# Kernel optimization log

Measured on AMD Instinct MI355X. Metric: run time of the kernel, lower is better.

The kernel has to match this reference:

```python
import jax, jax.numpy as jnp
import numpy as np

EPS = 1e-12  # torch F.normalize eps


def setup_inputs() -> dict:
    key = jax.random.key(0)
    k1, k2, k3, k4, k5 = jax.random.split(key, 5)
    N, C, H, W = 32, 512, 32, 32
    E = 1024   # expansion * dim
    G = 8      # group
    D = E // G # 128, per-group channel dim
    K = 64     # num_clusters
    x = jax.random.normal(k1, (N, C, H, W), dtype=jnp.float32)
    W1 = jax.random.normal(k2, (E, C), dtype=jnp.float32) / np.sqrt(C)
    W2 = jax.random.normal(k3, (G, E), dtype=jnp.float32) / np.sqrt(E)
    Wc = jax.random.normal(k4, (K, D), dtype=jnp.float32) / np.sqrt(D)
    centroids = jax.random.uniform(k5, (K, D), dtype=jnp.float32)
    return {"x": x, "W1": W1, "W2": W2, "Wc": Wc, "centroids": centroids}


def reference(x, W1, W2, Wc, centroids):
    # x: [N, C, H, W]; W1: [E, C]; W2: [G, E]; Wc: [K, D]; centroids: [K, D]
    N, C, H, W = x.shape
    E = W1.shape[0]
    G = W2.shape[0]
    K, D = Wc.shape
    P = H * W
    # descriptor-wise L2 normalization over channel dim
    norm = jnp.linalg.norm(x, axis=1, keepdims=True)
    x = x / jnp.maximum(norm, EPS)
    # linear1 on channels: [N, E, P]
    xe = jnp.einsum('ncp,ec->nep', x.reshape(N, C, P), W1)
    # grouped features: [N, G, D, P]
    xg = xe.reshape(N, G, D, P)
    # attention gate: sigmoid(linear2)  -> [N, G, P]
    att = jax.nn.sigmoid(jnp.einsum('nep,ge->ngp', xe, W2))
    # 1x1 conv = per-pixel matmul with cluster weights -> [N, G, K, P]
    soft_assign = jax.nn.softmax(jnp.einsum('ngdp,kd->ngkp', xg, Wc), axis=2)
    # combined per-(cluster,pixel) weight
    w = soft_assign * att[:, :, None, :]  # [N, G, K, P]
    # NetVLAD residual aggregation, algebraically decomposed to avoid the
    # giant [N,G,K,D,P] intermediate:
    #   vlad[n,k,d] = sum_{g,p} w * xg  -  centroids[k,d] * sum_{g,p} w
    agg = jnp.einsum('ngkp,ngdp->nkd', w, xg)  # [N, K, D]
    wsum = w.sum(axis=(1, 3))                  # [N, K]
    vlad = agg - wsum[:, :, None] * centroids[None]  # [N, K, D]
    return vlad.reshape(N, K * D)
```

## Files before the change

### kernel.cpp

```cpp
#include <hip/hip_runtime.h>


#define N_  32
#define C_  512
#define P_  1024
#define E_  1024
#define G_  8
#define D_  128
#define K_  64

typedef __attribute__((ext_vector_type(8))) short bf16x8;
typedef __attribute__((ext_vector_type(4))) float f32x4;

__device__ __forceinline__ unsigned short f2b(float f) {
    union { float f; unsigned u; } v; v.f = f;
    unsigned r = (v.u + 0x7FFFu + ((v.u >> 16) & 1u)) >> 16;
    return (unsigned short)r;
}
__device__ __forceinline__ float b2f(unsigned short h) {
    union { unsigned u; float f; } v; v.u = ((unsigned)h) << 16;
    return v.f;
}

__device__ __forceinline__ void gl_lds16(const void* g, void* l) {
    __builtin_amdgcn_global_load_lds(
        (const __attribute__((address_space(1))) void*)g,
        (__attribute__((address_space(3))) void*)l, 16, 0, 0);
}

__global__ __launch_bounds__(256) void k0_prep(const float* __restrict__ W1,
                                               const float* __restrict__ Wc,
                                               unsigned short* __restrict__ W1b,
                                               unsigned short* __restrict__ Vb) {
    int bid = blockIdx.x;
    int t = threadIdx.x;
    int i0 = bid * 512 + t;
    W1b[i0]       = f2b(W1[i0]);
    W1b[i0 + 256] = f2b(W1[i0 + 256]);
    int ch = bid & 1, k = (bid >> 1) & 63, g = bid >> 7;
    int c = ch * 256 + t;
    float acc = 0.f;
    #pragma unroll 8
    for (int d = 0; d < 128; ++d)
        acc += Wc[k * 128 + d] * W1[(g * 128 + d) * C_ + c];
    Vb[(g * 64 + k) * C_ + c] = f2b(acc);
}

__global__ __launch_bounds__(256) void k1_norm_transpose(const float* __restrict__ x,
                                                         unsigned short* __restrict__ xhat_t) {
    __shared__ short xc[128 * 256];
    __shared__ float red[256];
    __shared__ float rn[64];
    int n = blockIdx.y;
    int p0 = blockIdx.x * 64;
    int t = threadIdx.x;
    int ps = t & 63, cs = t >> 6;

    float ss = 0.f;
    for (int i = 0; i < 128; ++i) {
        float v = x[((size_t)(n * C_ + cs * 128 + i)) * P_ + p0 + ps];
        ss += v * v;
        xc[i * 256 + t] = (short)f2b(v);
    }
    red[t] = ss;
    __syncthreads();
    if (t < 64) {
        float s = red[t] + red[64 + t] + red[128 + t] + red[192 + t];
        rn[t] = 1.0f / fmaxf(sqrtf(s), 1e-12f);
    }
    __syncthreads();

    float r = rn[ps];
    size_t base = ((size_t)(n * P_ + p0 + ps)) * C_ + cs * 128;
    #pragma unroll
    for (int jj = 0; jj < 16; ++jj) {
        bf16x8 o;
        #pragma unroll
        for (int j = 0; j < 8; ++j)
            o[j] = (short)f2b(b2f((unsigned short)xc[(jj * 8 + j) * 256 + t]) * r);
        *(bf16x8*)&xhat_t[base + jj * 8] = o;
    }
}

__global__ __launch_bounds__(256) void k2_gemm_xe(const unsigned short* __restrict__ W1b,
                                                  const unsigned short* __restrict__ xhat_t,
                                                  unsigned short* __restrict__ xe) {
    __shared__ __align__(16) short As[128 * 64];
    __shared__ __align__(16) short Bs[128 * 64];
    int n = blockIdx.y;
    int e0 = (blockIdx.x >> 3) * 128;
    int p0 = (blockIdx.x & 7) * 128;
    int t = threadIdx.x;
    int w = t >> 6, l = t & 63, q = l >> 4, l15 = l & 15;
    int wr = w >> 1, wc = w & 1;

    f32x4 acc[4][4];
    #pragma unroll
    for (int mi = 0; mi < 4; ++mi)
        #pragma unroll
        for (int ni = 0; ni < 4; ++ni)
            acc[mi][ni] = (f32x4){0.f, 0.f, 0.f, 0.f};

    for (int ks = 0; ks < 8; ++ks) {
        int k0 = ks * 64;
        #pragma unroll
        for (int i = 0; i < 4; ++i) {
            int ch = i * 256 + t;
            int row = ch >> 3, col = (ch & 7) * 8;
            gl_lds16(&W1b[(e0 + row) * C_ + k0 + col], &As[ch * 8]);
        }
        #pragma unroll
        for (int i = 0; i < 4; ++i) {
            int ch = i * 256 + t;
            int row = ch >> 3, col = (ch & 7) * 8;
            gl_lds16(&xhat_t[((size_t)(n * P_ + p0 + row)) * C_ + k0 + col], &Bs[ch * 8]);
        }
        __syncthreads();

        #pragma unroll
        for (int kk = 0; kk < 2; ++kk) {
            bf16x8 af[4], bf[4];
            #pragma unroll
            for (int mi = 0; mi < 4; ++mi)
                af[mi] = *(const bf16x8*)&As[(wr * 64 + mi * 16 + l15) * 64 + kk * 32 + q * 8];
            #pragma unroll
            for (int ni = 0; ni < 4; ++ni)
                bf[ni] = *(const bf16x8*)&Bs[(wc * 64 + ni * 16 + l15) * 64 + kk * 32 + q * 8];
            #pragma unroll
            for (int mi = 0; mi < 4; ++mi)
                #pragma unroll
                for (int ni = 0; ni < 4; ++ni)
                    acc[mi][ni] = __builtin_amdgcn_mfma_f32_16x16x32_bf16(af[mi], bf[ni], acc[mi][ni], 0, 0, 0);
        }
        __syncthreads();
    }

    #pragma unroll
    for (int mi = 0; mi < 4; ++mi) {
        #pragma unroll
        for (int ni = 0; ni < 4; ++ni) {
            #pragma unroll
            for (int r = 0; r < 4; ++r) {
                int e = e0 + wr * 64 + mi * 16 + q * 4 + r;
                int p = p0 + wc * 64 + ni * 16 + l15;
                xe[((size_t)(n * E_ + e)) * P_ + p] = f2b(acc[mi][ni][r]);
            }
        }
    }
}

__global__ __launch_bounds__(256) void k3a_att_part(const unsigned short* __restrict__ xe,
                                                    const float* __restrict__ W2,
                                                    float* __restrict__ att_part) {
    int n = blockIdx.y;
    int ec = blockIdx.x;
    int t = threadIdx.x;
    int e0 = ec * 64;
    f32x4 acc[8];
    #pragma unroll
    for (int g = 0; g < 8; ++g) acc[g] = (f32x4){0.f, 0.f, 0.f, 0.f};
    #pragma unroll 4
    for (int i = 0; i < 64; ++i) {
        int e = e0 + i;
        ushort4 v4 = *(const ushort4*)&xe[((size_t)(n * E_ + e)) * P_ + t * 4];
        f32x4 vf = {b2f(v4.x), b2f(v4.y), b2f(v4.z), b2f(v4.w)};
        #pragma unroll
        for (int g = 0; g < 8; ++g)
            acc[g] += vf * W2[g * E_ + e];
    }
    #pragma unroll
    for (int g = 0; g < 8; ++g)
        *(f32x4*)&att_part[(((size_t)(n * 16 + ec)) * 8 + g) * P_ + t * 4] = acc[g];
}

__global__ __launch_bounds__(256) void k3b_att_reduce(const float* __restrict__ att_part,
                                                      float* __restrict__ att_s) {
    int idx = blockIdx.x * 256 + threadIdx.x;
    int p = idx & 1023;
    int g = (idx >> 10) & 7;
    int n = idx >> 13;
    float s = 0.f;
    #pragma unroll
    for (int ec = 0; ec < 16; ++ec)
        s += att_part[(((size_t)(n * 16 + ec)) * 8 + g) * P_ + p];
    att_s[idx] = 1.0f / (1.0f + __expf(-s));
}

__global__ __launch_bounds__(256) void k4_assign_agg(const unsigned short* __restrict__ Vb,
                                                     const unsigned short* __restrict__ xhat_t,
                                                     const unsigned short* __restrict__ xe,
                                                     const float* __restrict__ att_s,
                                                     float* __restrict__ agg_part,
                                                     float* __restrict__ wsum_part) {
    __shared__ __align__(16) char smem[8192 + 16384 + 34816 + 17408];
    short* As2   = (short*)smem;
    short* Bs2   = (short*)(smem + 8192);
    short* xglds = (short*)(smem + 24576);
    short* wlds  = (short*)(smem + 59392);

    int g = blockIdx.x & 7, ph = blockIdx.x >> 3, n = blockIdx.y;
    int t = threadIdx.x;
    int w = t >> 6, l = t & 63, q = l >> 4, l15 = l & 15;

    f32x4 acc_a[4][2];
    #pragma unroll
    for (int mi = 0; mi < 4; ++mi)
        #pragma unroll
        for (int ni = 0; ni < 2; ++ni)
            acc_a[mi][ni] = (f32x4){0.f, 0.f, 0.f, 0.f};
    float wsp[16];
    #pragma unroll
    for (int j = 0; j < 16; ++j) wsp[j] = 0.f;

    for (int cc = 0; cc < 4; ++cc) {
        int p0c = ph * 512 + cc * 128;

        #pragma unroll
        for (int i = 0; i < 8; ++i) {
            int ch = i * 256 + t;
            int row = ch / 17, col = (ch % 17) * 8;
            gl_lds16(&xe[((size_t)(n * E_ + g * 128 + row)) * P_ + p0c + col], &xglds[ch * 8]);
        }
        if (t < 128) {
            int ch = 2048 + t;
            int row = ch / 17, col = (ch % 17) * 8;
            gl_lds16(&xe[((size_t)(n * E_ + g * 128 + row)) * P_ + p0c + col], &xglds[ch * 8]);
        }

        f32x4 acc_s[4][2];
        #pragma unroll
        for (int mi = 0; mi < 4; ++mi)
            #pragma unroll
            for (int ni = 0; ni < 2; ++ni)
                acc_s[mi][ni] = (f32x4){0.f, 0.f, 0.f, 0.f};

        for (int ks = 0; ks < 8; ++ks) {
            int k0 = ks * 64;
            #pragma unroll
            for (int i = 0; i < 2; ++i) {
                int ch = i * 256 + t;
                int row = ch >> 3, col = (ch & 7) * 8;
                gl_lds16(&Vb[(g * 64 + row) * C_ + k0 + col], &As2[ch * 8]);
            }
            #pragma unroll
            for (int i = 0; i < 4; ++i) {
                int ch = i * 256 + t;
                int row = ch >> 3, col = (ch & 7) * 8;
                gl_lds16(&xhat_t[((size_t)(n * P_ + p0c + row)) * C_ + k0 + col], &Bs2[ch * 8]);
            }
            __syncthreads();
            #pragma unroll
            for (int kk = 0; kk < 2; ++kk) {
                bf16x8 af[4], bf2[2];
                #pragma unroll
                for (int mi = 0; mi < 4; ++mi)
                    af[mi] = *(const bf16x8*)&As2[(mi * 16 + l15) * 64 + kk * 32 + q * 8];
                #pragma unroll
                for (int ni = 0; ni < 2; ++ni)
                    bf2[ni] = *(const bf16x8*)&Bs2[(w * 32 + ni * 16 + l15) * 64 + kk * 32 + q * 8];
                #pragma unroll
                for (int mi = 0; mi < 4; ++mi)
                    #pragma unroll
                    for (int ni = 0; ni < 2; ++ni)
                        acc_s[mi][ni] = __builtin_amdgcn_mfma_f32_16x16x32_bf16(af[mi], bf2[ni], acc_s[mi][ni], 0, 0, 0);
            }
            __syncthreads();
        }

        #pragma unroll
        for (int ni = 0; ni < 2; ++ni) {
            float m = -1e30f;
            #pragma unroll
            for (int mi = 0; mi < 4; ++mi)
                #pragma unroll
                for (int r = 0; r < 4; ++r)
                    m = fmaxf(m, acc_s[mi][ni][r]);
            m = fmaxf(m, __shfl_xor(m, 16));
            m = fmaxf(m, __shfl_xor(m, 32));
            float s = 0.f;
            #pragma unroll
            for (int mi = 0; mi < 4; ++mi)
                #pragma unroll
                for (int r = 0; r < 4; ++r) {
                    float e = __expf(acc_s[mi][ni][r] - m);
                    acc_s[mi][ni][r] = e;
                    s += e;
                }
            s += __shfl_xor(s, 16);
            s += __shfl_xor(s, 32);

            int pcol = p0c + w * 32 + ni * 16 + l15;
            float av = att_s[(((size_t)(n * G_ + g)) * P_) + pcol];
            float scale = av / s;

            #pragma unroll
            for (int mi = 0; mi < 4; ++mi)
                #pragma unroll
                for (int r = 0; r < 4; ++r) {
                    float wv = acc_s[mi][ni][r] * scale;
                    wsp[mi * 4 + r] += wv;
                    wlds[(mi * 16 + q * 4 + r) * 136 + (w * 32 + ni * 16 + l15)] = (short)f2b(wv);
                }
        }
        __syncthreads();

        #pragma unroll
        for (int pk = 0; pk < 4; ++pk) {
            bf16x8 a2[4], b2[2];
            #pragma unroll
            for (int mi = 0; mi < 4; ++mi)
                a2[mi] = *(const bf16x8*)&wlds[(mi * 16 + l15) * 136 + pk * 32 + q * 8];
            #pragma unroll
            for (int ni = 0; ni < 2; ++ni)
                b2[ni] = *(const bf16x8*)&xglds[(w * 32 + ni * 16 + l15) * 136 + pk * 32 + q * 8];
            #pragma unroll
            for (int mi = 0; mi < 4; ++mi)
                #pragma unroll
                for (int ni = 0; ni < 2; ++ni)
                    acc_a[mi][ni] = __builtin_amdgcn_mfma_f32_16x16x32_bf16(a2[mi], b2[ni], acc_a[mi][ni], 0, 0, 0);
        }
        __syncthreads();
    }

    size_t base = (((size_t)(n * G_ + g)) * 2 + ph) * 64;
    #pragma unroll
    for (int mi = 0; mi < 4; ++mi)
        #pragma unroll
        for (int ni = 0; ni < 2; ++ni)
            #pragma unroll
            for (int r = 0; r < 4; ++r) {
                int k = mi * 16 + q * 4 + r;
                int d = w * 32 + ni * 16 + l15;
                agg_part[(base + k) * 128 + d] = acc_a[mi][ni][r];
            }

    #pragma unroll
    for (int j = 0; j < 16; ++j) {
        float v = wsp[j];
        v += __shfl_xor(v, 1);
        v += __shfl_xor(v, 2);
        v += __shfl_xor(v, 4);
        v += __shfl_xor(v, 8);
        if (l15 == 0) {
            int k = (j >> 2) * 16 + q * 4 + (j & 3);
            wsum_part[((((size_t)(n * G_ + g)) * 2 + ph) * 4 + w) * 64 + k] = v;
        }
    }
}

__global__ __launch_bounds__(256) void k5_final(const float* __restrict__ agg_part,
                                                const float* __restrict__ wsum_part,
                                                const float* __restrict__ centroids,
                                                float* __restrict__ out) {
    int idx = blockIdx.x * 256 + threadIdx.x;
    int d = idx & 127;
    int k = (idx >> 7) & 63;
    int n = idx >> 13;
    float ws = 0.f;
    #pragma unroll
    for (int g = 0; g < 8; ++g)
        #pragma unroll
        for (int ph = 0; ph < 2; ++ph)
            #pragma unroll
            for (int w2 = 0; w2 < 4; ++w2)
                ws += wsum_part[((((size_t)(n * G_ + g)) * 2 + ph) * 4 + w2) * 64 + k];
    float agg = 0.f;
    #pragma unroll
    for (int g = 0; g < 8; ++g)
        #pragma unroll
        for (int ph = 0; ph < 2; ++ph)
            agg += agg_part[(((((size_t)(n * G_ + g)) * 2 + ph) * 64) + k) * 128 + d];
    out[idx] = agg - ws * centroids[k * 128 + d];
}

extern "C" void kernel_launch(void* const* d_in, const int* in_sizes, int n_in,
                              void* d_out, int out_size, void* d_ws, size_t ws_size,
                              hipStream_t stream) {
    const float* x         = (const float*)d_in[0];
    const float* W1        = (const float*)d_in[1];
    const float* W2        = (const float*)d_in[2];
    const float* Wc        = (const float*)d_in[3];
    const float* centroids = (const float*)d_in[4];
    float* out = (float*)d_out;

    char* ws = (char*)d_ws;
    unsigned short* W1b      = (unsigned short*)(ws + 0);
    unsigned short* Vb       = (unsigned short*)(ws + 1048576);
    unsigned short* xhat_t   = (unsigned short*)(ws + 1572864);
    unsigned short* xe       = (unsigned short*)(ws + 35127296);
    float*          att_s    = (float*)(ws + 102236160);
    float*          att_part = (float*)(ws + 103284736);
    float*          agg_part = (float*)(ws + 103284736);
    float*          wsum_part= (float*)(ws + 120061952);

    hipLaunchKernelGGL(k0_prep,        dim3(1024), dim3(256), 0, stream, W1, Wc, W1b, Vb);
    hipLaunchKernelGGL(k1_norm_transpose, dim3(16, 32), dim3(256), 0, stream, x, xhat_t);
    hipLaunchKernelGGL(k2_gemm_xe,     dim3(64, 32), dim3(256), 0, stream, W1b, xhat_t, xe);
    hipLaunchKernelGGL(k3a_att_part,   dim3(16, 32), dim3(256), 0, stream, xe, W2, att_part);
    hipLaunchKernelGGL(k3b_att_reduce, dim3(1024), dim3(256), 0, stream, att_part, att_s);
    hipLaunchKernelGGL(k4_assign_agg,  dim3(16, 32), dim3(256), 0, stream, Vb, xhat_t, xe,
                       att_s, agg_part, wsum_part);
    hipLaunchKernelGGL(k5_final,       dim3(1024), dim3(256), 0, stream,
                       agg_part, wsum_part, centroids, out);
}
```

Baseline: 253.6 us.

## Fuse attention partials into xe GEMM epilogue and retile assign-aggregate kernel

The attention projection is now computed in the k2 GEMM epilogue from accumulator registers, so the separate pass that re-read all of xe is gone. k4 splits the pixel range into quarters, doubling the grid, and uses smaller K-step and xe tiles that alias shared memory, cutting LDS use to raise occupancy. A small kernel pre-reduces wsum so k5 does less redundant work. The costs are more partial aggregates for k5 to sum and extra epilogue shuffles and LDS traffic in k2.

```diff
diff --git a/kernel.cpp b/kernel.cpp
--- a/kernel.cpp
+++ b/kernel.cpp
@@ -84,7 +84,9 @@
 
 __global__ __launch_bounds__(256) void k2_gemm_xe(const unsigned short* __restrict__ W1b,
                                                   const unsigned short* __restrict__ xhat_t,
-                                                  unsigned short* __restrict__ xe) {
+                                                  const float* __restrict__ W2,
+                                                  unsigned short* __restrict__ xe,
+                                                  float* __restrict__ att_part) {
     __shared__ __align__(16) short As[128 * 64];
     __shared__ __align__(16) short Bs[128 * 64];
     int n = blockIdx.y;
@@ -147,30 +149,39 @@
             }
         }
     }
-}
-
-__global__ __launch_bounds__(256) void k3a_att_part(const unsigned short* __restrict__ xe,
-                                                    const float* __restrict__ W2,
-                                                    float* __restrict__ att_part) {
-    int n = blockIdx.y;
-    int ec = blockIdx.x;
-    int t = threadIdx.x;
-    int e0 = ec * 64;
-    f32x4 acc[8];
-    #pragma unroll
-    for (int g = 0; g < 8; ++g) acc[g] = (f32x4){0.f, 0.f, 0.f, 0.f};
-    #pragma unroll 4
-    for (int i = 0; i < 64; ++i) {
-        int e = e0 + i;
-        ushort4 v4 = *(const ushort4*)&xe[((size_t)(n * E_ + e)) * P_ + t * 4];
-        f32x4 vf = {b2f(v4.x), b2f(v4.y), b2f(v4.z), b2f(v4.w)};
-        #pragma unroll
-        for (int g = 0; g < 8; ++g)
-            acc[g] += vf * W2[g * E_ + e];
-    }
-    #pragma unroll
-    for (int g = 0; g < 8; ++g)
-        *(f32x4*)&att_part[(((size_t)(n * 16 + ec)) * 8 + g) * P_ + t * 4] = acc[g];
+
+    float* w2l = (float*)As;
+    #pragma unroll
+    for (int i = 0; i < 4; ++i) {
+        int idx = i * 256 + t;
+        w2l[idx] = W2[(idx >> 7) * E_ + e0 + (idx & 127)];
+    }
+    __syncthreads();
+    int slot = (blockIdx.x >> 3) * 2 + wr;
+    #pragma unroll
+    for (int gg = 0; gg < 8; ++gg) {
+        float pa[4] = {0.f, 0.f, 0.f, 0.f};
+        #pragma unroll
+        for (int mi = 0; mi < 4; ++mi)
+            #pragma unroll
+            for (int r = 0; r < 4; ++r) {
+                float w2v = w2l[gg * 128 + wr * 64 + mi * 16 + q * 4 + r];
+                #pragma unroll
+                for (int ni = 0; ni < 4; ++ni)
+                    pa[ni] += acc[mi][ni][r] * w2v;
+            }
+        #pragma unroll
+        for (int ni = 0; ni < 4; ++ni) {
+            pa[ni] += __shfl_xor(pa[ni], 16);
+            pa[ni] += __shfl_xor(pa[ni], 32);
+        }
+        if (q == 0) {
+            size_t ab = (((size_t)(n * 16 + slot)) * 8 + gg) * P_ + p0 + wc * 64;
+            #pragma unroll
+            for (int ni = 0; ni < 4; ++ni)
+                att_part[ab + ni * 16 + l15] = pa[ni];
+        }
+    }
 }
 
 __global__ __launch_bounds__(256) void k3b_att_reduce(const float* __restrict__ att_part,
@@ -181,8 +192,8 @@
     int n = idx >> 13;
     float s = 0.f;
     #pragma unroll
-    for (int ec = 0; ec < 16; ++ec)
-        s += att_part[(((size_t)(n * 16 + ec)) * 8 + g) * P_ + p];
+    for (int sl = 0; sl < 16; ++sl)
+        s += att_part[(((size_t)(n * 16 + sl)) * 8 + g) * P_ + p];
     att_s[idx] = 1.0f / (1.0f + __expf(-s));
 }
 
@@ -192,13 +203,14 @@
                                                      const float* __restrict__ att_s,
                                                      float* __restrict__ agg_part,
                                                      float* __restrict__ wsum_part) {
-    __shared__ __align__(16) char smem[8192 + 16384 + 34816 + 17408];
+    __shared__ __align__(16) char smem[18432 + 17408];
     short* As2   = (short*)smem;
-    short* Bs2   = (short*)(smem + 8192);
-    short* xglds = (short*)(smem + 24576);
-    short* wlds  = (short*)(smem + 59392);
-
-    int g = blockIdx.x & 7, ph = blockIdx.x >> 3, n = blockIdx.y;
+    short* Bs2   = (short*)(smem + 4096);
+    short* xglds = (short*)smem;
+    short* wlds  = (short*)(smem + 18432);
+
+    int bx = blockIdx.x;
+    int qt = bx & 3, g = bx >> 2, n = blockIdx.y;
     int t = threadIdx.x;
     int w = t >> 6, l = t & 63, q = l >> 4, l15 = l & 15;
 
@@ -212,20 +224,8 @@
     #pragma unroll
     for (int j = 0; j < 16; ++j) wsp[j] = 0.f;
 
-    for (int cc = 0; cc < 4; ++cc) {
-        int p0c = ph * 512 + cc * 128;
-
-        #pragma unroll
-        for (int i = 0; i < 8; ++i) {
-            int ch = i * 256 + t;
-            int row = ch / 17, col = (ch % 17) * 8;
-            gl_lds16(&xe[((size_t)(n * E_ + g * 128 + row)) * P_ + p0c + col], &xglds[ch * 8]);
-        }
-        if (t < 128) {
-            int ch = 2048 + t;
-            int row = ch / 17, col = (ch % 17) * 8;
-            gl_lds16(&xe[((size_t)(n * E_ + g * 128 + row)) * P_ + p0c + col], &xglds[ch * 8]);
-        }
+    for (int cc = 0; cc < 2; ++cc) {
+        int p0c = qt * 256 + cc * 128;
 
         f32x4 acc_s[4][2];
         #pragma unroll
@@ -234,36 +234,31 @@
             for (int ni = 0; ni < 2; ++ni)
                 acc_s[mi][ni] = (f32x4){0.f, 0.f, 0.f, 0.f};
 
-        for (int ks = 0; ks < 8; ++ks) {
-            int k0 = ks * 64;
+        for (int ks = 0; ks < 16; ++ks) {
+            int k0 = ks * 32;
+            {
+                int row = t >> 2, col = (t & 3) * 8;
+                gl_lds16(&Vb[(g * 64 + row) * C_ + k0 + col], &As2[t * 8]);
+            }
             #pragma unroll
             for (int i = 0; i < 2; ++i) {
                 int ch = i * 256 + t;
-                int row = ch >> 3, col = (ch & 7) * 8;
-                gl_lds16(&Vb[(g * 64 + row) * C_ + k0 + col], &As2[ch * 8]);
-            }
-            #pragma unroll
-            for (int i = 0; i < 4; ++i) {
-                int ch = i * 256 + t;
-                int row = ch >> 3, col = (ch & 7) * 8;
+                int row = ch >> 2, col = (ch & 3) * 8;
                 gl_lds16(&xhat_t[((size_t)(n * P_ + p0c + row)) * C_ + k0 + col], &Bs2[ch * 8]);
             }
             __syncthreads();
-            #pragma unroll
-            for (int kk = 0; kk < 2; ++kk) {
-                bf16x8 af[4], bf2[2];
-                #pragma unroll
-                for (int mi = 0; mi < 4; ++mi)
-                    af[mi] = *(const bf16x8*)&As2[(mi * 16 + l15) * 64 + kk * 32 + q * 8];
+            bf16x8 af[4], bf2[2];
+            #pragma unroll
+            for (int mi = 0; mi < 4; ++mi)
+                af[mi] = *(const bf16x8*)&As2[(mi * 16 + l15) * 32 + q * 8];
+            #pragma unroll
+            for (int ni = 0; ni < 2; ++ni)
+                bf2[ni] = *(const bf16x8*)&Bs2[(w * 32 + ni * 16 + l15) * 32 + q * 8];
+            #pragma unroll
+            for (int mi = 0; mi < 4; ++mi)
                 #pragma unroll
                 for (int ni = 0; ni < 2; ++ni)
-                    bf2[ni] = *(const bf16x8*)&Bs2[(w * 32 + ni * 16 + l15) * 64 + kk * 32 + q * 8];
-                #pragma unroll
-                for (int mi = 0; mi < 4; ++mi)
-                    #pragma unroll
-                    for (int ni = 0; ni < 2; ++ni)
-                        acc_s[mi][ni] = __builtin_amdgcn_mfma_f32_16x16x32_bf16(af[mi], bf2[ni], acc_s[mi][ni], 0, 0, 0);
-            }
+                    acc_s[mi][ni] = __builtin_amdgcn_mfma_f32_16x16x32_bf16(af[mi], bf2[ni], acc_s[mi][ni], 0, 0, 0);
             __syncthreads();
         }
 
@@ -302,27 +297,43 @@
                     wlds[(mi * 16 + q * 4 + r) * 136 + (w * 32 + ni * 16 + l15)] = (short)f2b(wv);
                 }
         }
-        __syncthreads();
-
-        #pragma unroll
-        for (int pk = 0; pk < 4; ++pk) {
-            bf16x8 a2[4], b2[2];
-            #pragma unroll
-            for (int mi = 0; mi < 4; ++mi)
-                a2[mi] = *(const bf16x8*)&wlds[(mi * 16 + l15) * 136 + pk * 32 + q * 8];
-            #pragma unroll
-            for (int ni = 0; ni < 2; ++ni)
-                b2[ni] = *(const bf16x8*)&xglds[(w * 32 + ni * 16 + l15) * 136 + pk * 32 + q * 8];
-            #pragma unroll
-            for (int mi = 0; mi < 4; ++mi)
+
+        for (int h = 0; h < 2; ++h) {
+            #pragma unroll
+            for (int i = 0; i < 4; ++i) {
+                int ch = i * 256 + t;
+                int row = ch / 9, col = (ch % 9) * 8;
+                gl_lds16(&xe[((size_t)(n * E_ + g * 128 + row)) * P_ + p0c + h * 64 + col],
+                         &xglds[ch * 8]);
+            }
+            if (t < 128) {
+                int ch = 1024 + t;
+                int row = ch / 9, col = (ch % 9) * 8;
+                gl_lds16(&xe[((size_t)(n * E_ + g * 128 + row)) * P_ + p0c + h * 64 + col],
+                         &xglds[ch * 8]);
+            }
+            __syncthreads();
+
+            #pragma unroll
+            for (int pk = 0; pk < 2; ++pk) {
+                bf16x8 a2[4], b2[2];
+                #pragma unroll
+                for (int mi = 0; mi < 4; ++mi)
+                    a2[mi] = *(const bf16x8*)&wlds[(mi * 16 + l15) * 136 + h * 64 + pk * 32 + q * 8];
                 #pragma unroll
                 for (int ni = 0; ni < 2; ++ni)
-                    acc_a[mi][ni] = __builtin_amdgcn_mfma_f32_16x16x32_bf16(a2[mi], b2[ni], acc_a[mi][ni], 0, 0, 0);
-        }
-        __syncthreads();
-    }
-
-    size_t base = (((size_t)(n * G_ + g)) * 2 + ph) * 64;
+                    b2[ni] = *(const bf16x8*)&xglds[(w * 32 + ni * 16 + l15) * 72 + pk * 32 + q * 8];
+                #pragma unroll
+                for (int mi = 0; mi < 4; ++mi)
+                    #pragma unroll
+                    for (int ni = 0; ni < 2; ++ni)
+                        acc_a[mi][ni] = __builtin_amdgcn_mfma_f32_16x16x32_bf16(a2[mi], b2[ni], acc_a[mi][ni], 0, 0, 0);
+            }
+            __syncthreads();
+        }
+    }
+
+    size_t base = (((size_t)(n * G_ + g)) * 4 + qt) * 64;
     #pragma unroll
     for (int mi = 0; mi < 4; ++mi)
         #pragma unroll
@@ -343,34 +354,41 @@
         v += __shfl_xor(v, 8);
         if (l15 == 0) {
             int k = (j >> 2) * 16 + q * 4 + (j & 3);
-            wsum_part[((((size_t)(n * G_ + g)) * 2 + ph) * 4 + w) * 64 + k] = v;
-        }
-    }
+            wsum_part[(base + 0) * 0 + ((((size_t)(n * G_ + g)) * 4 + qt) * 4 + w) * 64 + k] = v;
+        }
+    }
+}
+
+__global__ __launch_bounds__(256) void k4c_wsum(const float* __restrict__ wsum_part,
+                                                float* __restrict__ wsum) {
+    int idx = blockIdx.x * 256 + threadIdx.x;
+    int n = idx >> 6, k = idx & 63;
+    float s = 0.f;
+    #pragma unroll
+    for (int g = 0; g < 8; ++g)
+        #pragma unroll
+        for (int qt = 0; qt < 4; ++qt)
+            #pragma unroll
+            for (int w2 = 0; w2 < 4; ++w2)
+                s += wsum_part[((((size_t)(n * G_ + g)) * 4 + qt) * 4 + w2) * 64 + k];
+    wsum[idx] = s;
 }
 
 __global__ __launch_bounds__(256) void k5_final(const float* __restrict__ agg_part,
-                                                const float* __restrict__ wsum_part,
+                                                const float* __restrict__ wsum,
                                                 const float* __restrict__ centroids,
                                                 float* __restrict__ out) {
     int idx = blockIdx.x * 256 + threadIdx.x;
     int d = idx & 127;
     int k = (idx >> 7) & 63;
     int n = idx >> 13;
-    float ws = 0.f;
+    float ag = 0.f;
     #pragma unroll
     for (int g = 0; g < 8; ++g)
         #pragma unroll
-        for (int ph = 0; ph < 2; ++ph)
-            #pragma unroll
-            for (int w2 = 0; w2 < 4; ++w2)
-                ws += wsum_part[((((size_t)(n * G_ + g)) * 2 + ph) * 4 + w2) * 64 + k];
-    float agg = 0.f;
-    #pragma unroll
-    for (int g = 0; g < 8; ++g)
-        #pragma unroll
-        for (int ph = 0; ph < 2; ++ph)
-            agg += agg_part[(((((size_t)(n * G_ + g)) * 2 + ph) * 64) + k) * 128 + d];
-    out[idx] = agg - ws * centroids[k * 128 + d];
+        for (int qt = 0; qt < 4; ++qt)
+            ag += agg_part[((((size_t)(n * G_ + g)) * 4 + qt) * 64 + k) * 128 + d];
+    out[idx] = ag - wsum[n * 64 + k] * centroids[k * 128 + d];
 }
 
 extern "C" void kernel_launch(void* const* d_in, const int* in_sizes, int n_in,
@@ -391,15 +409,17 @@
     float*          att_s    = (float*)(ws + 102236160);
     float*          att_part = (float*)(ws + 103284736);
     float*          agg_part = (float*)(ws + 103284736);
-    float*          wsum_part= (float*)(ws + 120061952);
+    float*          wsum_part= (float*)(ws + 136839168);
+    float*          wsum     = (float*)(ws + 138936320);
 
     hipLaunchKernelGGL(k0_prep,        dim3(1024), dim3(256), 0, stream, W1, Wc, W1b, Vb);
     hipLaunchKernelGGL(k1_norm_transpose, dim3(16, 32), dim3(256), 0, stream, x, xhat_t);
-    hipLaunchKernelGGL(k2_gemm_xe,     dim3(64, 32), dim3(256), 0, stream, W1b, xhat_t, xe);
-    hipLaunchKernelGGL(k3a_att_part,   dim3(16, 32), dim3(256), 0, stream, xe, W2, att_part);
+    hipLaunchKernelGGL(k2_gemm_xe,     dim3(64, 32), dim3(256), 0, stream,
+                       W1b, xhat_t, W2, xe, att_part);
     hipLaunchKernelGGL(k3b_att_reduce, dim3(1024), dim3(256), 0, stream, att_part, att_s);
-    hipLaunchKernelGGL(k4_assign_agg,  dim3(16, 32), dim3(256), 0, stream, Vb, xhat_t, xe,
+    hipLaunchKernelGGL(k4_assign_agg,  dim3(32, 32), dim3(256), 0, stream, Vb, xhat_t, xe,
                        att_s, agg_part, wsum_part);
+    hipLaunchKernelGGL(k4c_wsum,       dim3(8), dim3(256), 0, stream, wsum_part, wsum);
     hipLaunchKernelGGL(k5_final,       dim3(1024), dim3(256), 0, stream,
-                       agg_part, wsum_part, centroids, out);
-}
+                       agg_part, wsum, centroids, out);
+}
```

Measured after the change: 264.8 us. 4.5% more time.
